# Kernel optimization log

Hardware: AMD Instinct MI355X
Metric: run time of the kernel (lower is better)

## Reference

```python
import jax, jax.numpy as jnp
import numpy as np

B, T, C = 4, 2048, 1024
H, D = 16, 64  # n_heads, head_dim; C == H*D

def setup_inputs() -> dict:
    key = jax.random.key(0)
    ks = jax.random.split(key, 6)
    s_in = 1.0 / np.sqrt(C)
    x = jax.random.normal(ks[0], (B, T, C), dtype=jnp.float32)
    # causal mask: True above the diagonal -> masked to -inf
    mask = jnp.triu(jnp.ones((T, T), dtype=bool), k=1)
    Wqkv = jax.random.uniform(ks[1], (C, 3 * C), jnp.float32, -s_in, s_in)
    bqkv = jax.random.uniform(ks[2], (3 * C,), jnp.float32, -s_in, s_in)
    Wout = jax.random.uniform(ks[3], (C, C), jnp.float32, -s_in, s_in)
    bout = jax.random.uniform(ks[4], (C,), jnp.float32, -s_in, s_in)
    return {"x": x, "mask": mask, "Wqkv": Wqkv, "bqkv": bqkv, "Wout": Wout, "bout": bout}

def reference(x, mask, Wqkv, bqkv, Wout, bout):
    b, t, c = x.shape
    qkv = (x @ Wqkv + bqkv).reshape(b, t, 3, H, D)
    qkv = jnp.transpose(qkv, (2, 0, 3, 1, 4))  # [3, B, H, T, D]
    q, k, v = qkv[0], qkv[1], qkv[2]
    scores = jnp.einsum("bhqd,bhkd->bhqk", q, k) / jnp.sqrt(jnp.float32(D))
    scores = jnp.where(mask[:t, :t][None, None, :, :], -jnp.inf, scores)
    attn = jax.nn.softmax(scores, axis=-1)
    out = jnp.einsum("bhqk,bhkd->bhqd", attn, v)
    out = jnp.transpose(out, (0, 2, 1, 3)).reshape(b, t, c)
    return out @ Wout + bout
```

## Files before the change

kernel.cpp:

```cpp
#include <hip/hip_runtime.h>

typedef unsigned short u16;
typedef __attribute__((ext_vector_type(8))) short bf16x8;
typedef __attribute__((ext_vector_type(4))) short bf16x4;
typedef __attribute__((ext_vector_type(4))) float f32x4;

#define MFMA16(a, b, c) __builtin_amdgcn_mfma_f32_16x16x32_bf16(a, b, c, 0, 0, 0)

__device__ __forceinline__ u16 f2bf(float x) {
    unsigned u = __float_as_uint(x);
    return (u16)((u + 0x7fffu + ((u >> 16) & 1u)) >> 16);
}
__device__ __forceinline__ u16 f2bf_fast(float x) {
    return (u16)((__float_as_uint(x) + 0x8000u) >> 16);
}

__global__ __launch_bounds__(256) void castk(const float* __restrict__ src, u16* __restrict__ dst) {
    const int i = (blockIdx.x * 256 + threadIdx.x) * 8;
    float4 a = *(const float4*)(src + i);
    float4 b = *(const float4*)(src + i + 4);
    bf16x8 v;
    v[0] = (short)f2bf(a.x); v[1] = (short)f2bf(a.y);
    v[2] = (short)f2bf(a.z); v[3] = (short)f2bf(a.w);
    v[4] = (short)f2bf(b.x); v[5] = (short)f2bf(b.y);
    v[6] = (short)f2bf(b.z); v[7] = (short)f2bf(b.w);
    *(bf16x8*)(dst + i) = v;
}

__global__ __launch_bounds__(256) void tkern(const float* __restrict__ src, u16* __restrict__ dst,
                                             int R, int C) {
    const int tC = C >> 6;
    const int tr = (blockIdx.x / tC) << 6;
    const int tc = (blockIdx.x % tC) << 6;
    __shared__ u16 ls[64 * 68];
    const int tid = threadIdx.x;
#pragma unroll
    for (int rep = 0; rep < 2; ++rep) {
        const int f = tid * 8 + rep * 2048;
        const int r = f >> 6, c = f & 63;
        float4 a = *(const float4*)(src + (size_t)(tr + r) * C + tc + c);
        float4 b = *(const float4*)(src + (size_t)(tr + r) * C + tc + c + 4);
        bf16x4 lo, hi;
        lo[0] = (short)f2bf(a.x); lo[1] = (short)f2bf(a.y);
        lo[2] = (short)f2bf(a.z); lo[3] = (short)f2bf(a.w);
        hi[0] = (short)f2bf(b.x); hi[1] = (short)f2bf(b.y);
        hi[2] = (short)f2bf(b.z); hi[3] = (short)f2bf(b.w);
        *(bf16x4*)&ls[r * 68 + c] = lo;
        *(bf16x4*)&ls[r * 68 + c + 4] = hi;
    }
    __syncthreads();
#pragma unroll
    for (int rep = 0; rep < 2; ++rep) {
        const int f = tid * 8 + rep * 2048;
        const int rn = f >> 6, ck = f & 63;
        bf16x8 v;
#pragma unroll
        for (int j = 0; j < 8; ++j) v[j] = (short)ls[(ck + j) * 68 + rn];
        *(bf16x8*)(dst + (size_t)(tc + rn) * R + tr + ck) = v;
    }
}

template <int MODE>
__global__ __launch_bounds__(256) void gemm_k(const u16* __restrict__ A, const u16* __restrict__ Bt,
                                              const float* __restrict__ bias,
                                              u16* __restrict__ Qo, u16* __restrict__ Ko,
                                              u16* __restrict__ Vo, float* __restrict__ Of) {
    constexpr int Kd = 1024;
    const int tid = threadIdx.x;
    const int lane = tid & 63, wave = tid >> 6;
    const int wm = wave >> 1, wn = wave & 1;
    const int lr = lane & 15, lg = lane >> 4;
    const int mt = blockIdx.x & 63;
    const int nt = blockIdx.x >> 6;
    const int mbase = mt << 7, nbase = nt << 7;
    __shared__ u16 As[128 * 32];
    __shared__ u16 Bs[128 * 32];
    f32x4 acc[4][4];
#pragma unroll
    for (int i = 0; i < 4; ++i)
#pragma unroll
        for (int j = 0; j < 4; ++j) acc[i][j] = {0.f, 0.f, 0.f, 0.f};

    for (int kb = 0; kb < Kd; kb += 32) {
        __syncthreads();
#pragma unroll
        for (int rep = 0; rep < 2; ++rep) {
            const int f = tid * 8 + rep * 2048;
            const int r = f >> 5, c = f & 31;
            __builtin_amdgcn_global_load_lds(
                (const __attribute__((address_space(1))) void*)(A + (size_t)(mbase + r) * Kd + kb + c),
                (__attribute__((address_space(3))) void*)(As + f), 16, 0, 0);
            __builtin_amdgcn_global_load_lds(
                (const __attribute__((address_space(1))) void*)(Bt + (size_t)(nbase + r) * Kd + kb + c),
                (__attribute__((address_space(3))) void*)(Bs + f), 16, 0, 0);
        }
        __syncthreads();
        bf16x8 af[4], bfr[4];
#pragma unroll
        for (int i = 0; i < 4; ++i)
            af[i] = *(const bf16x8*)&As[(wm * 64 + i * 16 + lr) * 32 + lg * 8];
#pragma unroll
        for (int j = 0; j < 4; ++j)
            bfr[j] = *(const bf16x8*)&Bs[(wn * 64 + j * 16 + lr) * 32 + lg * 8];
#pragma unroll
        for (int i = 0; i < 4; ++i)
#pragma unroll
            for (int j = 0; j < 4; ++j) acc[i][j] = MFMA16(af[i], bfr[j], acc[i][j]);
    }

    const float QSCALE = 0.1803368801111137f;
#pragma unroll
    for (int j = 0; j < 4; ++j) {
        const int n = nbase + wn * 64 + j * 16 + lr;
        const float bj = bias[n];
        if (MODE == 0) {
            const int three = n >> 10;
            const int h = (n >> 6) & 15;
            const int d = n & 63;
#pragma unroll
            for (int i = 0; i < 4; ++i) {
#pragma unroll
                for (int r = 0; r < 4; ++r) {
                    const int m = mbase + wm * 64 + i * 16 + lg * 4 + r;
                    const int b = m >> 11, t = m & 2047;
                    const int bh = (b << 4) + h;
                    const float val = acc[i][j][r] + bj;
                    if (three == 0)
                        Qo[(((size_t)bh << 11) + t) * 64 + d] = f2bf(val * QSCALE);
                    else if (three == 1)
                        Ko[(((size_t)bh << 11) + t) * 64 + d] = f2bf(val);
                    else
                        Vo[(((size_t)bh << 6) + d) * 2048 + t] = f2bf(val);
                }
            }
        } else {
#pragma unroll
            for (int i = 0; i < 4; ++i) {
#pragma unroll
                for (int r = 0; r < 4; ++r) {
                    const int m = mbase + wm * 64 + i * 16 + lg * 4 + r;
                    Of[((size_t)m << 10) + n] = acc[i][j][r] + bj;
                }
            }
        }
    }
}

__global__ __launch_bounds__(256) void flash_attn(const u16* __restrict__ Q, const u16* __restrict__ Kg,
                                                  const u16* __restrict__ Vt, u16* __restrict__ Aout) {
    const int tid = threadIdx.x;
    const int lane = tid & 63, wave = tid >> 6;
    const int lr = lane & 15, lg = lane >> 4;
    const int bx = blockIdx.x;
    const int bh = blockIdx.y;
    const int b = bh >> 4, h = bh & 15;
    const size_t base = (size_t)bh << 17;

    const int qb_hi = 16 + bx;
    const int qb_lo = 15 - bx;

    __shared__ u16 Ks[64 * 64];
    __shared__ u16 Vs[64 * 64];
    __shared__ u16 Ps[4][16 * 72];

    int qbase[2];
    qbase[0] = qb_hi * 64 + wave * 16;
    qbase[1] = qb_lo * 64 + wave * 16;

    bf16x8 qf[2][2];
#pragma unroll
    for (int st = 0; st < 2; ++st) {
        const u16* p = Q + base + (size_t)(qbase[st] + lr) * 64;
        qf[st][0] = *(const bf16x8*)(p + lg * 8);
        qf[st][1] = *(const bf16x8*)(p + 32 + lg * 8);
    }

    f32x4 o[2][4];
#pragma unroll
    for (int st = 0; st < 2; ++st)
#pragma unroll
        for (int dt = 0; dt < 4; ++dt) o[st][dt] = {0.f, 0.f, 0.f, 0.f};
    float m_[2] = {-INFINITY, -INFINITY};
    float l_[2] = {0.f, 0.f};

    const int f0 = tid * 16;
    const int row0 = f0 >> 7, c0 = (f0 >> 4) & 7;
    const int cc0 = c0 ^ (row0 & 7);
    const int f1 = (tid + 256) * 16;
    const int row1 = f1 >> 7, c1 = (f1 >> 4) & 7;
    const int cc1 = c1 ^ (row1 & 7);

    const int xr = lr & 7;

    auto process = [&](int st, bool diag, int kt) {
        f32x4 s[4];
#pragma unroll
        for (int rt = 0; rt < 4; ++rt) {
            const int krow = rt * 16 + lr;
            const bf16x8 k0 = *(const bf16x8*)&Ks[krow * 64 + ((lg) ^ xr) * 8];
            const bf16x8 k1 = *(const bf16x8*)&Ks[krow * 64 + ((lg + 4) ^ xr) * 8];
            f32x4 z = {0.f, 0.f, 0.f, 0.f};
            z = MFMA16(k0, qf[st][0], z);
            z = MFMA16(k1, qf[st][1], z);
            s[rt] = z;
        }
        if (diag) {
            const int q_glob = qbase[st] + lr;
#pragma unroll
            for (int rt = 0; rt < 4; ++rt)
#pragma unroll
                for (int r = 0; r < 4; ++r) {
                    const int kv = kt * 64 + rt * 16 + lg * 4 + r;
                    if (kv > q_glob) s[rt][r] = -INFINITY;
                }
        }
        float rmax = -INFINITY;
#pragma unroll
        for (int rt = 0; rt < 4; ++rt)
#pragma unroll
            for (int r = 0; r < 4; ++r) rmax = fmaxf(rmax, s[rt][r]);
        rmax = fmaxf(rmax, __shfl_xor(rmax, 16));
        rmax = fmaxf(rmax, __shfl_xor(rmax, 32));
        const float m_new = fmaxf(m_[st], rmax);
        const float alpha = exp2f(m_[st] - m_new);
        float rsum = 0.f;
#pragma unroll
        for (int rt = 0; rt < 4; ++rt)
#pragma unroll
            for (int r = 0; r < 4; ++r) {
                const float p = exp2f(s[rt][r] - m_new);
                s[rt][r] = p;
                rsum += p;
            }
        rsum += __shfl_xor(rsum, 16);
        rsum += __shfl_xor(rsum, 32);
        l_[st] = l_[st] * alpha + rsum;
        m_[st] = m_new;

        u16* psb = &Ps[wave][0];
#pragma unroll
        for (int rt = 0; rt < 4; ++rt) {
            bf16x4 pk;
#pragma unroll
            for (int r = 0; r < 4; ++r) pk[r] = (short)f2bf_fast(s[rt][r]);
            *(bf16x4*)&psb[lr * 72 + rt * 16 + lg * 4] = pk;
        }
        float aq[4];
#pragma unroll
        for (int r = 0; r < 4; ++r) aq[r] = __shfl(alpha, (lane & 48) + lg * 4 + r);
#pragma unroll
        for (int dt = 0; dt < 4; ++dt)
#pragma unroll
            for (int r = 0; r < 4; ++r) o[st][dt][r] *= aq[r];

        const bf16x8 pf0 = *(const bf16x8*)&psb[lr * 72 + lg * 8];
        const bf16x8 pf1 = *(const bf16x8*)&psb[lr * 72 + 32 + lg * 8];
#pragma unroll
        for (int dt = 0; dt < 4; ++dt) {
            const int vrow = dt * 16 + lr;
            const bf16x8 v0 = *(const bf16x8*)&Vs[vrow * 64 + ((lg) ^ xr) * 8];
            const bf16x8 v1 = *(const bf16x8*)&Vs[vrow * 64 + ((lg + 4) ^ xr) * 8];
            o[st][dt] = MFMA16(pf0, v0, o[st][dt]);
            o[st][dt] = MFMA16(pf1, v1, o[st][dt]);
        }
    };

    for (int kt = 0; kt <= qb_hi; ++kt) {
        __syncthreads();
        __builtin_amdgcn_global_load_lds(
            (const __attribute__((address_space(1))) void*)(Kg + base + (size_t)(kt * 64 + row0) * 64 + cc0 * 8),
            (__attribute__((address_space(3))) void*)(Ks + tid * 8), 16, 0, 0);
        __builtin_amdgcn_global_load_lds(
            (const __attribute__((address_space(1))) void*)(Kg + base + (size_t)(kt * 64 + row1) * 64 + cc1 * 8),
            (__attribute__((address_space(3))) void*)(Ks + 2048 + tid * 8), 16, 0, 0);
        __builtin_amdgcn_global_load_lds(
            (const __attribute__((address_space(1))) void*)(Vt + base + (size_t)row0 * 2048 + kt * 64 + cc0 * 8),
            (__attribute__((address_space(3))) void*)(Vs + tid * 8), 16, 0, 0);
        __builtin_amdgcn_global_load_lds(
            (const __attribute__((address_space(1))) void*)(Vt + base + (size_t)row1 * 2048 + kt * 64 + cc1 * 8),
            (__attribute__((address_space(3))) void*)(Vs + 2048 + tid * 8), 16, 0, 0);
        __syncthreads();

        process(0, kt == qb_hi, kt);
        if (kt <= qb_lo) process(1, kt == qb_lo, kt);
    }

#pragma unroll
    for (int st = 0; st < 2; ++st) {
        const float linv = 1.f / l_[st];
        float lq[4];
#pragma unroll
        for (int r = 0; r < 4; ++r) lq[r] = __shfl(linv, (lane & 48) + lg * 4 + r);
#pragma unroll
        for (int dt = 0; dt < 4; ++dt)
#pragma unroll
            for (int r = 0; r < 4; ++r) {
                const int t = qbase[st] + lg * 4 + r;
                Aout[(((size_t)(b << 11) + t) << 10) + h * 64 + dt * 16 + lr] =
                    f2bf(o[st][dt][r] * lq[r]);
            }
    }
}

extern "C" void kernel_launch(void* const* d_in, const int* in_sizes, int n_in,
                              void* d_out, int out_size, void* d_ws, size_t ws_size,
                              hipStream_t stream) {
    (void)in_sizes; (void)n_in; (void)out_size; (void)ws_size;
    const float* x    = (const float*)d_in[0];
    const float* Wqkv = (const float*)d_in[2];
    const float* bqkv = (const float*)d_in[3];
    const float* Wout = (const float*)d_in[4];
    const float* bout = (const float*)d_in[5];
    float* out = (float*)d_out;

    char* ws = (char*)d_ws;
    u16* WqkvT = (u16*)(ws);
    u16* WoutT = (u16*)(ws + 6291456);
    u16* xb    = (u16*)(ws + 8388608);
    u16* Qb    = (u16*)(ws + 25165824);
    u16* Kb    = (u16*)(ws + 41943040);
    u16* Vtb   = (u16*)(ws + 58720256);
    u16* Ab    = (u16*)(ws + 75497472);

    castk<<<dim3(4096), 256, 0, stream>>>(x, xb);
    tkern<<<dim3(16 * 48), 256, 0, stream>>>(Wqkv, WqkvT, 1024, 3072);
    tkern<<<dim3(16 * 16), 256, 0, stream>>>(Wout, WoutT, 1024, 1024);
    gemm_k<0><<<dim3(64 * 24), 256, 0, stream>>>(xb, WqkvT, bqkv, Qb, Kb, Vtb, nullptr);
    flash_attn<<<dim3(16, 64), 256, 0, stream>>>(Qb, Kb, Vtb, Ab);
    gemm_k<1><<<dim3(64 * 8), 256, 0, stream>>>(Ab, WoutT, bout, nullptr, nullptr, nullptr, out);
}
```

Before: 329.1 us.

## Double-buffer K/V tiles in flash attention and swizzle blocks across XCDs

The K/V LDS tiles become double buffered, so the next tile's global-to-LDS loads are issued before the current tile is processed, and one barrier per iteration is removed. The 2D grid becomes a 1D grid with a block-index swizzle, so the query blocks of one batch-head land on the same XCD and share its L2 for K/V. The padded P scratch buffer is replaced by an XOR-swizzled unpadded layout to avoid LDS bank conflicts. LDS use roughly doubles, which may lower occupancy.

```diff
diff --git a/kernel.cpp b/kernel.cpp
--- a/kernel.cpp
+++ b/kernel.cpp
@@ -151,17 +151,19 @@
     const int tid = threadIdx.x;
     const int lane = tid & 63, wave = tid >> 6;
     const int lr = lane & 15, lg = lane >> 4;
-    const int bx = blockIdx.x;
-    const int bh = blockIdx.y;
+    const int bid = blockIdx.x;
+    const int swz = (bid & 7) * 128 + (bid >> 3);
+    const int bh = swz >> 4;
+    const int bx = swz & 15;
     const int b = bh >> 4, h = bh & 15;
     const size_t base = (size_t)bh << 17;
 
     const int qb_hi = 16 + bx;
     const int qb_lo = 15 - bx;
 
-    __shared__ u16 Ks[64 * 64];
-    __shared__ u16 Vs[64 * 64];
-    __shared__ u16 Ps[4][16 * 72];
+    __shared__ u16 Ks[2][64 * 64];
+    __shared__ u16 Vs[2][64 * 64];
+    __shared__ u16 Ps[4][16 * 64];
 
     int qbase[2];
     qbase[0] = qb_hi * 64 + wave * 16;
@@ -192,13 +194,29 @@
 
     const int xr = lr & 7;
 
-    auto process = [&](int st, bool diag, int kt) {
+    auto stage = [&](int sel, int kt) {
+        const size_t krow = base + (size_t)(kt * 64) * 64;
+        __builtin_amdgcn_global_load_lds(
+            (const __attribute__((address_space(1))) void*)(Kg + krow + (size_t)row0 * 64 + cc0 * 8),
+            (__attribute__((address_space(3))) void*)(&Ks[sel][tid * 8]), 16, 0, 0);
+        __builtin_amdgcn_global_load_lds(
+            (const __attribute__((address_space(1))) void*)(Kg + krow + (size_t)row1 * 64 + cc1 * 8),
+            (__attribute__((address_space(3))) void*)(&Ks[sel][2048 + tid * 8]), 16, 0, 0);
+        __builtin_amdgcn_global_load_lds(
+            (const __attribute__((address_space(1))) void*)(Vt + base + (size_t)row0 * 2048 + kt * 64 + cc0 * 8),
+            (__attribute__((address_space(3))) void*)(&Vs[sel][tid * 8]), 16, 0, 0);
+        __builtin_amdgcn_global_load_lds(
+            (const __attribute__((address_space(1))) void*)(Vt + base + (size_t)row1 * 2048 + kt * 64 + cc1 * 8),
+            (__attribute__((address_space(3))) void*)(&Vs[sel][2048 + tid * 8]), 16, 0, 0);
+    };
+
+    auto process = [&](int sel, int st, bool diag, int kt) {
         f32x4 s[4];
 #pragma unroll
         for (int rt = 0; rt < 4; ++rt) {
             const int krow = rt * 16 + lr;
-            const bf16x8 k0 = *(const bf16x8*)&Ks[krow * 64 + ((lg) ^ xr) * 8];
-            const bf16x8 k1 = *(const bf16x8*)&Ks[krow * 64 + ((lg + 4) ^ xr) * 8];
+            const bf16x8 k0 = *(const bf16x8*)&Ks[sel][krow * 64 + ((lg) ^ xr) * 8];
+            const bf16x8 k1 = *(const bf16x8*)&Ks[sel][krow * 64 + ((lg + 4) ^ xr) * 8];
             f32x4 z = {0.f, 0.f, 0.f, 0.f};
             z = MFMA16(k0, qf[st][0], z);
             z = MFMA16(k1, qf[st][1], z);
@@ -243,7 +261,7 @@
             bf16x4 pk;
 #pragma unroll
             for (int r = 0; r < 4; ++r) pk[r] = (short)f2bf_fast(s[rt][r]);
-            *(bf16x4*)&psb[lr * 72 + rt * 16 + lg * 4] = pk;
+            *(bf16x4*)&psb[lr * 64 + (((rt * 2 + (lg >> 1)) ^ xr) << 3) + ((lg & 1) << 2)] = pk;
         }
         float aq[4];
 #pragma unroll
@@ -253,36 +271,25 @@
 #pragma unroll
             for (int r = 0; r < 4; ++r) o[st][dt][r] *= aq[r];
 
-        const bf16x8 pf0 = *(const bf16x8*)&psb[lr * 72 + lg * 8];
-        const bf16x8 pf1 = *(const bf16x8*)&psb[lr * 72 + 32 + lg * 8];
+        const bf16x8 pf0 = *(const bf16x8*)&psb[lr * 64 + ((lg ^ xr) << 3)];
+        const bf16x8 pf1 = *(const bf16x8*)&psb[lr * 64 + (((4 + lg) ^ xr) << 3)];
 #pragma unroll
         for (int dt = 0; dt < 4; ++dt) {
             const int vrow = dt * 16 + lr;
-            const bf16x8 v0 = *(const bf16x8*)&Vs[vrow * 64 + ((lg) ^ xr) * 8];
-            const bf16x8 v1 = *(const bf16x8*)&Vs[vrow * 64 + ((lg + 4) ^ xr) * 8];
+            const bf16x8 v0 = *(const bf16x8*)&Vs[sel][vrow * 64 + ((lg) ^ xr) * 8];
+            const bf16x8 v1 = *(const bf16x8*)&Vs[sel][vrow * 64 + ((lg + 4) ^ xr) * 8];
             o[st][dt] = MFMA16(pf0, v0, o[st][dt]);
             o[st][dt] = MFMA16(pf1, v1, o[st][dt]);
         }
     };
 
+    stage(0, 0);
     for (int kt = 0; kt <= qb_hi; ++kt) {
+        const int cur = kt & 1;
         __syncthreads();
-        __builtin_amdgcn_global_load_lds(
-            (const __attribute__((address_space(1))) void*)(Kg + base + (size_t)(kt * 64 + row0) * 64 + cc0 * 8),
-            (__attribute__((address_space(3))) void*)(Ks + tid * 8), 16, 0, 0);
-        __builtin_amdgcn_global_load_lds(
-            (const __attribute__((address_space(1))) void*)(Kg + base + (size_t)(kt * 64 + row1) * 64 + cc1 * 8),
-            (__attribute__((address_space(3))) void*)(Ks + 2048 + tid * 8), 16, 0, 0);
-        __builtin_amdgcn_global_load_lds(
-            (const __attribute__((address_space(1))) void*)(Vt + base + (size_t)row0 * 2048 + kt * 64 + cc0 * 8),
-            (__attribute__((address_space(3))) void*)(Vs + tid * 8), 16, 0, 0);
-        __builtin_amdgcn_global_load_lds(
-            (const __attribute__((address_space(1))) void*)(Vt + base + (size_t)row1 * 2048 + kt * 64 + cc1 * 8),
-            (__attribute__((address_space(3))) void*)(Vs + 2048 + tid * 8), 16, 0, 0);
-        __syncthreads();
-
-        process(0, kt == qb_hi, kt);
-        if (kt <= qb_lo) process(1, kt == qb_lo, kt);
+        if (kt < qb_hi) stage(cur ^ 1, kt + 1);
+        process(cur, 0, kt == qb_hi, kt);
+        if (kt <= qb_lo) process(cur, 1, kt == qb_lo, kt);
     }
 
 #pragma unroll
@@ -326,6 +333,6 @@
     tkern<<<dim3(16 * 48), 256, 0, stream>>>(Wqkv, WqkvT, 1024, 3072);
     tkern<<<dim3(16 * 16), 256, 0, stream>>>(Wout, WoutT, 1024, 1024);
     gemm_k<0><<<dim3(64 * 24), 256, 0, stream>>>(xb, WqkvT, bqkv, Qb, Kb, Vtb, nullptr);
-    flash_attn<<<dim3(16, 64), 256, 0, stream>>>(Qb, Kb, Vtb, Ab);
+    flash_attn<<<dim3(1024), 256, 0, stream>>>(Qb, Kb, Vtb, Ab);
     gemm_k<1><<<dim3(64 * 8), 256, 0, stream>>>(Ab, WoutT, bout, nullptr, nullptr, nullptr, out);
 }
```

Measured after the change: 320.8 us. 1.03x faster.
